# Performance work log

Hardware: AMD Instinct MI355X
Metric: run time of the kernel (lower is better)

## Reference

```python
import jax, jax.numpy as jnp
import numpy as np

B, T, I, H = 64, 1024, 256, 256  # batch, seq, input_size, hidden_size
L, D = 2, 2                      # num_layers, num_directions (bidirectional)


def setup_inputs() -> dict:
    key = jax.random.key(0)
    ks = jax.random.split(key, 10)
    s = 0.1
    return {
        "inputs": jax.random.normal(ks[0], (B, T, I), dtype=jnp.float32),
        "hidden_state": jnp.zeros((L * D, B, H), dtype=jnp.float32),  # unused by module
        # layer 0: input size I;  layer 1: input size D*H (bidirectional concat)
        "w_ih0": jax.random.normal(ks[1], (D, 4 * H, I), dtype=jnp.float32) * s,
        "w_hh0": jax.random.normal(ks[2], (D, 4 * H, H), dtype=jnp.float32) * s,
        "b_ih0": jax.random.normal(ks[3], (D, 4 * H), dtype=jnp.float32) * s,
        "b_hh0": jax.random.normal(ks[4], (D, 4 * H), dtype=jnp.float32) * s,
        "w_ih1": jax.random.normal(ks[5], (D, 4 * H, D * H), dtype=jnp.float32) * s,
        "w_hh1": jax.random.normal(ks[6], (D, 4 * H, H), dtype=jnp.float32) * s,
        "b_ih1": jax.random.normal(ks[7], (D, 4 * H), dtype=jnp.float32) * s,
        "b_hh1": jax.random.normal(ks[8], (D, 4 * H), dtype=jnp.float32) * s,
    }


def _lstm_dir(x, w_ih, w_hh, b_ih, b_hh, reverse):
    # x: [B,T,F]; PyTorch gate order: i, f, g, o
    xg = jnp.einsum('btf,gf->btg', x, w_ih) + b_ih + b_hh  # [B,T,4H], input GEMM hoisted
    xg = jnp.swapaxes(xg, 0, 1)  # [T,B,4H]
    Hs = w_hh.shape[1]
    bsz = x.shape[0]

    def step(carry, g_t):
        h, c = carry
        g = g_t + h @ w_hh.T
        i, f, gg, o = jnp.split(g, 4, axis=-1)
        c = jax.nn.sigmoid(f) * c + jax.nn.sigmoid(i) * jnp.tanh(gg)
        h = jax.nn.sigmoid(o) * jnp.tanh(c)
        return (h, c), h

    init = (jnp.zeros((bsz, Hs), x.dtype), jnp.zeros((bsz, Hs), x.dtype))
    (hT, cT), ys = jax.lax.scan(step, init, xg, reverse=reverse)
    return jnp.swapaxes(ys, 0, 1), hT, cT  # [B,T,H], [B,H], [B,H]


def _bilstm(x, w_ih, w_hh, b_ih, b_hh):
    of, hf, cf = _lstm_dir(x, w_ih[0], w_hh[0], b_ih[0], b_hh[0], False)
    ob, hb, cb = _lstm_dir(x, w_ih[1], w_hh[1], b_ih[1], b_hh[1], True)
    out = jnp.concatenate([of, ob], axis=-1)        # [B,T,2H]
    h_n = jnp.stack([hf, hb], axis=0)               # [2,B,H]
    c_n = jnp.stack([cf, cb], axis=0)
    return out, h_n, c_n


def reference(inputs, hidden_state, w_ih0, w_hh0, b_ih0, b_hh0,
              w_ih1, w_hh1, b_ih1, b_hh1):
    # hidden_state is accepted but ignored, matching the original module
    o1, h1, c1 = _bilstm(inputs, w_ih0, w_hh0, b_ih0, b_hh0)
    o2, h2, c2 = _bilstm(o1, w_ih1, w_hh1, b_ih1, b_hh1)
    h_n = jnp.concatenate([h1, h2], axis=0)  # [4,B,H]
    c_n = jnp.concatenate([c1, c2], axis=0)
    return o2, (h_n, c_n)
```

## Files before the change

kernel.cpp:

```cpp
#include <hip/hip_runtime.h>
#include <hip/hip_fp16.h>


#define BQ 64
#define TT 1024
#define II 256
#define M0 (BQ * TT)
#define G4 4

typedef _Float16 half8 __attribute__((ext_vector_type(8)));
typedef float floatx4 __attribute__((ext_vector_type(4)));

__device__ __forceinline__ float fsig(float x) {
  float e = __builtin_amdgcn_exp2f(-1.44269504089f * x);
  return __builtin_amdgcn_rcpf(1.0f + e);
}
__device__ __forceinline__ float ftanh(float x) {
  float ax = __builtin_fabsf(x);
  float e = __builtin_amdgcn_exp2f(-2.88539008178f * ax);
  float r = (1.0f - e) * __builtin_amdgcn_rcpf(1.0f + e);
  return __builtin_copysignf(r, x);
}
__device__ __forceinline__ half8 cvt8(float4 a, float4 b) {
  half8 h;
  h[0] = (_Float16)a.x; h[1] = (_Float16)a.y; h[2] = (_Float16)a.z; h[3] = (_Float16)a.w;
  h[4] = (_Float16)b.x; h[5] = (_Float16)b.y; h[6] = (_Float16)b.z; h[7] = (_Float16)b.w;
  return h;
}

__global__ __launch_bounds__(256) void pack_xT(const float* __restrict__ x,
                                               _Float16* __restrict__ xT) {
  int gid = blockIdx.x * 256 + threadIdx.x;
  int chunk = gid & 31;
  int row = gid >> 5;
  int t = row >> 6, b = row & 63;
  const float* src = x + ((size_t)b * TT + t) * II + chunk * 8;
  float4 v0 = *(const float4*)src;
  float4 v1 = *(const float4*)(src + 4);
  *(half8*)(xT + (size_t)row * II + chunk * 8) = cvt8(v0, v1);
}

__global__ __launch_bounds__(256) void pack_B(const float* __restrict__ W,
                                              _Float16* __restrict__ dst, int K,
                                              int total) {
  int gid = blockIdx.x * 256 + threadIdx.x;
  if (gid >= total) return;
  int per = 64 * (K / 32) * 64;
  int d = gid / per;
  int i = gid - d * per;
  int lane = i & 63;
  int i2 = i >> 6;
  int n = (i2 / (K / 32)) * 16 + (lane & 15);
  int k = (i2 % (K / 32)) * 32 + (lane >> 4) * 8;
  const float* s = W + ((size_t)d * 1024 + n) * K + k;
  float4 v0 = *(const float4*)s;
  float4 v1 = *(const float4*)(s + 4);
  *(half8*)(dst + (size_t)gid * 8) = cvt8(v0, v1);
}

__global__ __launch_bounds__(256) void add_bias(const float* __restrict__ a,
                                                const float* __restrict__ b,
                                                float* __restrict__ o, int n) {
  int i = blockIdx.x * 256 + threadIdx.x;
  if (i < n) o[i] = a[i] + b[i];
}

template <int K>
__global__ __launch_bounds__(256) void gemm_xg(const _Float16* __restrict__ A,
                                               const _Float16* __restrict__ Bp,
                                               const float* __restrict__ bias,
                                               _Float16* __restrict__ out) {
  const int d = blockIdx.z;
  const int n0 = blockIdx.x * 128;
  const int m0 = blockIdx.y * 128;
  const int tid = threadIdx.x;
  const int lane = tid & 63, wave = tid >> 6;
  const int wr = wave >> 1, wc = wave & 1;
  const int cl = lane & 15, lh = lane >> 4;
  __shared__ _Float16 As[128][48];
  const _Float16* Bb = Bp + (size_t)d * (1024 * K);
  floatx4 acc[4][4];
#pragma unroll
  for (int i = 0; i < 4; i++)
#pragma unroll
    for (int j = 0; j < 4; j++) acc[i][j] = (floatx4){0.f, 0.f, 0.f, 0.f};

  for (int ks = 0; ks < K / 32; ++ks) {
#pragma unroll
    for (int it = 0; it < 2; ++it) {
      int row = it * 64 + (tid >> 2);
      int col = (tid & 3) * 8;
      *(half8*)(&As[row][col]) =
          *(const half8*)(A + (size_t)(m0 + row) * K + ks * 32 + col);
    }
    __syncthreads();
    half8 a[4], b[4];
#pragma unroll
    for (int rt = 0; rt < 4; rt++)
      a[rt] = *(const half8*)(&As[wr * 64 + rt * 16 + cl][lh * 8]);
#pragma unroll
    for (int ct = 0; ct < 4; ct++) {
      int tile = (n0 >> 4) + wc * 4 + ct;
      b[ct] = *(const half8*)(Bb + ((size_t)(tile * (K / 32) + ks) * 64 + lane) * 8);
    }
#pragma unroll
    for (int rt = 0; rt < 4; rt++)
#pragma unroll
      for (int ct = 0; ct < 4; ct++)
        acc[rt][ct] = __builtin_amdgcn_mfma_f32_16x16x32_f16(a[rt], b[ct], acc[rt][ct], 0, 0, 0);
    __syncthreads();
  }
#pragma unroll
  for (int ct = 0; ct < 4; ct++) {
    int n = n0 + wc * 64 + ct * 16 + cl;
    float bv = bias[d * 1024 + n];
#pragma unroll
    for (int rt = 0; rt < 4; rt++) {
      int mb = m0 + wr * 64 + rt * 16 + lh * 4;
#pragma unroll
      for (int r = 0; r < 4; r++)
        out[(size_t)d * ((size_t)M0 * 1024) + (size_t)(mb + r) * 1024 + n] =
            (_Float16)(acc[rt][ct][r] + bv);
    }
  }
}

template <int LAYER>
__global__ __launch_bounds__(512, 2) void lstm_rec(
    const _Float16* __restrict__ xg, const _Float16* __restrict__ Whp,
    _Float16* __restrict__ o1, float* __restrict__ out,
    _Float16* __restrict__ hx, unsigned* __restrict__ ctr) {
  const int wg = blockIdx.x;
  const int dir = wg >> 2, s = wg & 3;
  const int tid = threadIdx.x;
  const int lane = tid & 63, wave = tid >> 6;
  const int cl = lane & 15, lh = lane >> 4;
  const int wr = wave >> 2, wc = wave & 3;
  const int j = s * 64 + wc * 16 + cl;
  const int pair = LAYER * 2 + dir;
  unsigned* myctr = ctr + pair;
  _Float16* buf0 = hx + (size_t)(pair * 2 + 0) * (64 * 256);
  _Float16* buf1 = hx + (size_t)(pair * 2 + 1) * (64 * 256);
  const size_t o2elems = (size_t)BQ * TT * 512;

  const _Float16* Wb = Whp + (size_t)dir * (1024 * 256);
  half8 w[4][8];
#pragma unroll
  for (int g = 0; g < 4; g++) {
    const int tile = g * 16 + s * 4 + wc;
#pragma unroll
    for (int ks = 0; ks < 8; ks++)
      w[g][ks] = *(const half8*)(Wb + ((size_t)(tile * 8 + ks) * 64 + lane) * 8);
  }
  float c[2][4];
#pragma unroll
  for (int mi = 0; mi < 2; mi++)
#pragma unroll
    for (int r = 0; r < 4; r++) c[mi][r] = 0.f;

  for (int t = 0; t < TT; ++t) {
    const int tt = dir ? (TT - 1 - t) : t;
    const _Float16* xgrow = xg + ((size_t)dir * M0 + (size_t)tt * BQ) * 1024;
    float xf[2][4][4];
#pragma unroll
    for (int mi = 0; mi < 2; mi++)
#pragma unroll
      for (int g = 0; g < 4; g++)
#pragma unroll
        for (int r = 0; r < 4; r++)
          xf[mi][g][r] =
              (float)xgrow[(size_t)((wr * 2 + mi) * 16 + lh * 4 + r) * 1024 + g * 256 + j];

    if (tid == 0) {
      const unsigned target = (unsigned)(G4 * t);
      while (__hip_atomic_load(myctr, __ATOMIC_RELAXED, __HIP_MEMORY_SCOPE_AGENT) <
             target) {
        __builtin_amdgcn_s_sleep(1);
      }
      __threadfence();
    }
    __syncthreads();

    const _Float16* hr = (t & 1) ? buf1 : buf0;
    floatx4 acc[2][4];
#pragma unroll
    for (int mi = 0; mi < 2; mi++)
#pragma unroll
      for (int g = 0; g < 4; g++) acc[mi][g] = (floatx4){0.f, 0.f, 0.f, 0.f};
#pragma unroll
    for (int ks = 0; ks < 8; ks++) {
      half8 a0 = *(const half8*)(hr + (size_t)((wr * 2 + 0) * 16 + cl) * 256 + ks * 32 + lh * 8);
      half8 a1 = *(const half8*)(hr + (size_t)((wr * 2 + 1) * 16 + cl) * 256 + ks * 32 + lh * 8);
#pragma unroll
      for (int g = 0; g < 4; g++) {
        acc[0][g] = __builtin_amdgcn_mfma_f32_16x16x32_f16(a0, w[g][ks], acc[0][g], 0, 0, 0);
        acc[1][g] = __builtin_amdgcn_mfma_f32_16x16x32_f16(a1, w[g][ks], acc[1][g], 0, 0, 0);
      }
    }

    _Float16* hw = (t & 1) ? buf0 : buf1;
#pragma unroll
    for (int mi = 0; mi < 2; mi++)
#pragma unroll
      for (int r = 0; r < 4; r++) {
        float gi = acc[mi][0][r] + xf[mi][0][r];
        float gf = acc[mi][1][r] + xf[mi][1][r];
        float gg = acc[mi][2][r] + xf[mi][2][r];
        float go = acc[mi][3][r] + xf[mi][3][r];
        float cc = fsig(gf) * c[mi][r] + fsig(gi) * ftanh(gg);
        c[mi][r] = cc;
        float h = fsig(go) * ftanh(cc);
        const int b = (wr * 2 + mi) * 16 + lh * 4 + r;
        hw[(size_t)b * 256 + j] = (_Float16)h;
        if (LAYER == 0) {
          o1[((size_t)tt * BQ + b) * 512 + dir * 256 + j] = (_Float16)h;
        } else {
          out[((size_t)b * TT + tt) * 512 + dir * 256 + j] = h;
        }
        if (t == TT - 1) {
          const int row = LAYER * 2 + dir;
          out[o2elems + ((size_t)row * BQ + b) * 256 + j] = h;
          out[o2elems + (size_t)4 * BQ * 256 + ((size_t)row * BQ + b) * 256 + j] = cc;
        }
      }

    __syncthreads();
    if (tid == 0)
      __hip_atomic_fetch_add(myctr, 1u, __ATOMIC_RELEASE, __HIP_MEMORY_SCOPE_AGENT);
  }
}

extern "C" void kernel_launch(void* const* d_in, const int* in_sizes, int n_in,
                              void* d_out, int out_size, void* d_ws, size_t ws_size,
                              hipStream_t stream) {
  (void)in_sizes; (void)n_in; (void)out_size; (void)ws_size;
  const float* x = (const float*)d_in[0];
  const float* wih0 = (const float*)d_in[2];
  const float* whh0 = (const float*)d_in[3];
  const float* bih0 = (const float*)d_in[4];
  const float* bhh0 = (const float*)d_in[5];
  const float* wih1 = (const float*)d_in[6];
  const float* whh1 = (const float*)d_in[7];
  const float* bih1 = (const float*)d_in[8];
  const float* bhh1 = (const float*)d_in[9];
  float* out = (float*)d_out;

  char* p = (char*)d_ws;
  unsigned* ctr = (unsigned*)p;   p += 256;
  _Float16* hx = (_Float16*)p;    p += (size_t)4 * 2 * 64 * 256 * 2;
  _Float16* xT = (_Float16*)p;    p += (size_t)M0 * II * 2;
  _Float16* o1 = (_Float16*)p;    p += (size_t)M0 * 512 * 2;
  _Float16* xgb = (_Float16*)p;   p += (size_t)2 * M0 * 1024 * 2;
  _Float16* pwih0 = (_Float16*)p; p += (size_t)2 * 1024 * 256 * 2;
  _Float16* pwhh0 = (_Float16*)p; p += (size_t)2 * 1024 * 256 * 2;
  _Float16* pwih1 = (_Float16*)p; p += (size_t)2 * 1024 * 512 * 2;
  _Float16* pwhh1 = (_Float16*)p; p += (size_t)2 * 1024 * 256 * 2;
  float* bias0 = (float*)p;       p += 2 * 1024 * 4;
  float* bias1 = (float*)p;       p += 2 * 1024 * 4;

  hipMemsetAsync(d_ws, 0, 256 + (size_t)4 * 2 * 64 * 256 * 2, stream);

  hipLaunchKernelGGL(pack_xT, dim3(8192), dim3(256), 0, stream, x, xT);
  hipLaunchKernelGGL(pack_B, dim3(256), dim3(256), 0, stream, wih0, pwih0, 256, 2 * 1024 * 256 / 8);
  hipLaunchKernelGGL(pack_B, dim3(256), dim3(256), 0, stream, whh0, pwhh0, 256, 2 * 1024 * 256 / 8);
  hipLaunchKernelGGL(pack_B, dim3(512), dim3(256), 0, stream, wih1, pwih1, 512, 2 * 1024 * 512 / 8);
  hipLaunchKernelGGL(pack_B, dim3(256), dim3(256), 0, stream, whh1, pwhh1, 256, 2 * 1024 * 256 / 8);
  hipLaunchKernelGGL(add_bias, dim3(8), dim3(256), 0, stream, bih0, bhh0, bias0, 2048);
  hipLaunchKernelGGL(add_bias, dim3(8), dim3(256), 0, stream, bih1, bhh1, bias1, 2048);

  hipLaunchKernelGGL((gemm_xg<256>), dim3(8, 512, 2), dim3(256), 0, stream, xT, pwih0, bias0, xgb);
  hipLaunchKernelGGL((lstm_rec<0>), dim3(8), dim3(512), 0, stream, xgb, pwhh0, o1, out, hx, ctr);
  hipLaunchKernelGGL((gemm_xg<512>), dim3(8, 512, 2), dim3(256), 0, stream, o1, pwih1, bias1, xgb);
  hipLaunchKernelGGL((lstm_rec<1>), dim3(8), dim3(512), 0, stream, xgb, pwhh1, (_Float16*)nullptr, out, hx, ctr);
}
```

Before: 17.48 ms.

## Use system-scope relaxed atomics for recurrent sync and gate-interleave xg layout

The input-projection GEMM now writes its gate preactivations in a layout where the four gates for each hidden unit are contiguous and grouped by slice, so the recurrent kernel fetches them with a single 8-byte load per row. The per-step barrier drops the __threadfence and acquire/release ordering. It relies instead on relaxed system-scope atomic loads and stores of the hidden-state buffer so that they bypass non-coherent caches. Counters are padded to separate 256-byte lines, and output stores use nontemporal hints. Without the release/acquire ordering, correctness depends on the hardware keeping these memory operations in order.

```diff
diff --git a/kernel.cpp b/kernel.cpp
--- a/kernel.cpp
+++ b/kernel.cpp
@@ -9,7 +9,9 @@
 #define G4 4
 
 typedef _Float16 half8 __attribute__((ext_vector_type(8)));
+typedef _Float16 half4 __attribute__((ext_vector_type(4)));
 typedef float floatx4 __attribute__((ext_vector_type(4)));
+typedef unsigned long long u64;
 
 __device__ __forceinline__ float fsig(float x) {
   float e = __builtin_amdgcn_exp2f(-1.44269504089f * x);
@@ -26,6 +28,9 @@
   h[0] = (_Float16)a.x; h[1] = (_Float16)a.y; h[2] = (_Float16)a.z; h[3] = (_Float16)a.w;
   h[4] = (_Float16)b.x; h[5] = (_Float16)b.y; h[6] = (_Float16)b.z; h[7] = (_Float16)b.w;
   return h;
+}
+__device__ __forceinline__ half8 h8_from(u64 lo, u64 hi) {
+  union { u64 u[2]; half8 v; } cv; cv.u[0] = lo; cv.u[1] = hi; return cv.v;
 }
 
 __global__ __launch_bounds__(256) void pack_xT(const float* __restrict__ x,
@@ -69,7 +74,7 @@
 __global__ __launch_bounds__(256) void gemm_xg(const _Float16* __restrict__ A,
                                                const _Float16* __restrict__ Bp,
                                                const float* __restrict__ bias,
-                                               _Float16* __restrict__ out) {
+                                               _Float16* __restrict__ xg2) {
   const int d = blockIdx.z;
   const int n0 = blockIdx.x * 128;
   const int m0 = blockIdx.y * 128;
@@ -113,21 +118,24 @@
 #pragma unroll
   for (int ct = 0; ct < 4; ct++) {
     int n = n0 + wc * 64 + ct * 16 + cl;
+    int g = n >> 8, sl = (n >> 6) & 3, jj = n & 63;
     float bv = bias[d * 1024 + n];
 #pragma unroll
     for (int rt = 0; rt < 4; rt++) {
-      int mb = m0 + wr * 64 + rt * 16 + lh * 4;
-#pragma unroll
-      for (int r = 0; r < 4; r++)
-        out[(size_t)d * ((size_t)M0 * 1024) + (size_t)(mb + r) * 1024 + n] =
+#pragma unroll
+      for (int r = 0; r < 4; r++) {
+        int m = m0 + wr * 64 + rt * 16 + lh * 4 + r;
+        int ttv = m >> 6, b = m & 63;
+        xg2[((((size_t)d * 1024 + ttv) * 4 + sl) * 64 + b) * 256 + jj * 4 + g] =
             (_Float16)(acc[rt][ct][r] + bv);
+      }
     }
   }
 }
 
 template <int LAYER>
 __global__ __launch_bounds__(512, 2) void lstm_rec(
-    const _Float16* __restrict__ xg, const _Float16* __restrict__ Whp,
+    const _Float16* __restrict__ xg2, const _Float16* __restrict__ Whp,
     _Float16* __restrict__ o1, float* __restrict__ out,
     _Float16* __restrict__ hx, unsigned* __restrict__ ctr) {
   const int wg = blockIdx.x;
@@ -136,9 +144,10 @@
   const int lane = tid & 63, wave = tid >> 6;
   const int cl = lane & 15, lh = lane >> 4;
   const int wr = wave >> 2, wc = wave & 3;
-  const int j = s * 64 + wc * 16 + cl;
+  const int jj = wc * 16 + cl;
+  const int j = s * 64 + jj;
   const int pair = LAYER * 2 + dir;
-  unsigned* myctr = ctr + pair;
+  unsigned* myctr = ctr + pair * 64;
   _Float16* buf0 = hx + (size_t)(pair * 2 + 0) * (64 * 256);
   _Float16* buf1 = hx + (size_t)(pair * 2 + 1) * (64 * 256);
   const size_t o2elems = (size_t)BQ * TT * 512;
@@ -160,24 +169,22 @@
 
   for (int t = 0; t < TT; ++t) {
     const int tt = dir ? (TT - 1 - t) : t;
-    const _Float16* xgrow = xg + ((size_t)dir * M0 + (size_t)tt * BQ) * 1024;
-    float xf[2][4][4];
+    const _Float16* xb = xg2 + ((((size_t)dir * TT + tt) * 4 + s) << 14);
+    u64 xraw[2][4];
 #pragma unroll
     for (int mi = 0; mi < 2; mi++)
 #pragma unroll
-      for (int g = 0; g < 4; g++)
-#pragma unroll
-        for (int r = 0; r < 4; r++)
-          xf[mi][g][r] =
-              (float)xgrow[(size_t)((wr * 2 + mi) * 16 + lh * 4 + r) * 1024 + g * 256 + j];
+      for (int r = 0; r < 4; r++) {
+        int b = wr * 32 + mi * 16 + lh * 4 + r;
+        xraw[mi][r] = *(const u64*)(xb + ((size_t)b * 64 + jj) * 4);
+      }
 
     if (tid == 0) {
       const unsigned target = (unsigned)(G4 * t);
-      while (__hip_atomic_load(myctr, __ATOMIC_RELAXED, __HIP_MEMORY_SCOPE_AGENT) <
-             target) {
+      while (__hip_atomic_load(myctr, __ATOMIC_RELAXED,
+                               __HIP_MEMORY_SCOPE_SYSTEM) < target) {
         __builtin_amdgcn_s_sleep(1);
       }
-      __threadfence();
     }
     __syncthreads();
 
@@ -189,8 +196,13 @@
       for (int g = 0; g < 4; g++) acc[mi][g] = (floatx4){0.f, 0.f, 0.f, 0.f};
 #pragma unroll
     for (int ks = 0; ks < 8; ks++) {
-      half8 a0 = *(const half8*)(hr + (size_t)((wr * 2 + 0) * 16 + cl) * 256 + ks * 32 + lh * 8);
-      half8 a1 = *(const half8*)(hr + (size_t)((wr * 2 + 1) * 16 + cl) * 256 + ks * 32 + lh * 8);
+      const _Float16* p0 = hr + (size_t)(wr * 32 + cl) * 256 + ks * 32 + lh * 8;
+      const _Float16* p1 = hr + (size_t)(wr * 32 + 16 + cl) * 256 + ks * 32 + lh * 8;
+      u64 a0l = __hip_atomic_load((const u64*)p0, __ATOMIC_RELAXED, __HIP_MEMORY_SCOPE_SYSTEM);
+      u64 a0h = __hip_atomic_load((const u64*)(p0 + 4), __ATOMIC_RELAXED, __HIP_MEMORY_SCOPE_SYSTEM);
+      u64 a1l = __hip_atomic_load((const u64*)p1, __ATOMIC_RELAXED, __HIP_MEMORY_SCOPE_SYSTEM);
+      u64 a1h = __hip_atomic_load((const u64*)(p1 + 4), __ATOMIC_RELAXED, __HIP_MEMORY_SCOPE_SYSTEM);
+      half8 a0 = h8_from(a0l, a0h), a1 = h8_from(a1l, a1h);
 #pragma unroll
       for (int g = 0; g < 4; g++) {
         acc[0][g] = __builtin_amdgcn_mfma_f32_16x16x32_f16(a0, w[g][ks], acc[0][g], 0, 0, 0);
@@ -203,19 +215,23 @@
     for (int mi = 0; mi < 2; mi++)
 #pragma unroll
       for (int r = 0; r < 4; r++) {
-        float gi = acc[mi][0][r] + xf[mi][0][r];
-        float gf = acc[mi][1][r] + xf[mi][1][r];
-        float gg = acc[mi][2][r] + xf[mi][2][r];
-        float go = acc[mi][3][r] + xf[mi][3][r];
+        union { u64 u; half4 h; } xc; xc.u = xraw[mi][r];
+        float gi = acc[mi][0][r] + (float)xc.h[0];
+        float gf = acc[mi][1][r] + (float)xc.h[1];
+        float gg = acc[mi][2][r] + (float)xc.h[2];
+        float go = acc[mi][3][r] + (float)xc.h[3];
         float cc = fsig(gf) * c[mi][r] + fsig(gi) * ftanh(gg);
         c[mi][r] = cc;
         float h = fsig(go) * ftanh(cc);
-        const int b = (wr * 2 + mi) * 16 + lh * 4 + r;
-        hw[(size_t)b * 256 + j] = (_Float16)h;
+        const int b = wr * 32 + mi * 16 + lh * 4 + r;
+        __hip_atomic_store(hw + (size_t)b * 256 + j, (_Float16)h,
+                           __ATOMIC_RELAXED, __HIP_MEMORY_SCOPE_SYSTEM);
         if (LAYER == 0) {
-          o1[((size_t)tt * BQ + b) * 512 + dir * 256 + j] = (_Float16)h;
+          __builtin_nontemporal_store((_Float16)h,
+              o1 + ((size_t)tt * BQ + b) * 512 + dir * 256 + j);
         } else {
-          out[((size_t)b * TT + tt) * 512 + dir * 256 + j] = h;
+          __builtin_nontemporal_store(h,
+              out + ((size_t)b * TT + tt) * 512 + dir * 256 + j);
         }
         if (t == TT - 1) {
           const int row = LAYER * 2 + dir;
@@ -226,7 +242,7 @@
 
     __syncthreads();
     if (tid == 0)
-      __hip_atomic_fetch_add(myctr, 1u, __ATOMIC_RELEASE, __HIP_MEMORY_SCOPE_AGENT);
+      __hip_atomic_fetch_add(myctr, 1u, __ATOMIC_RELAXED, __HIP_MEMORY_SCOPE_SYSTEM);
   }
 }
 
@@ -246,7 +262,7 @@
   float* out = (float*)d_out;
 
   char* p = (char*)d_ws;
-  unsigned* ctr = (unsigned*)p;   p += 256;
+  unsigned* ctr = (unsigned*)p;   p += 1024;
   _Float16* hx = (_Float16*)p;    p += (size_t)4 * 2 * 64 * 256 * 2;
   _Float16* xT = (_Float16*)p;    p += (size_t)M0 * II * 2;
   _Float16* o1 = (_Float16*)p;    p += (size_t)M0 * 512 * 2;
@@ -258,7 +274,7 @@
   float* bias0 = (float*)p;       p += 2 * 1024 * 4;
   float* bias1 = (float*)p;       p += 2 * 1024 * 4;
 
-  hipMemsetAsync(d_ws, 0, 256 + (size_t)4 * 2 * 64 * 256 * 2, stream);
+  hipMemsetAsync(d_ws, 0, 1024 + (size_t)4 * 2 * 64 * 256 * 2, stream);
 
   hipLaunchKernelGGL(pack_xT, dim3(8192), dim3(256), 0, stream, x, xT);
   hipLaunchKernelGGL(pack_B, dim3(256), dim3(256), 0, stream, wih0, pwih0, 256, 2 * 1024 * 256 / 8);
```

Result: slower. 23.86 ms (+36.5%).
